# Optimization experiments

Hardware: AMD Instinct MI355X
Metric: run time of the kernel (lower is better)

## Reference

```python
import jax, jax.numpy as jnp
import numpy as np
from jax import lax

B, C, H, W, E = 16, 256, 64, 64, 4
KH = KW = 3
EPS = 1e-5  # torch BatchNorm2d default


def conv2d(x, w, groups=1):
    # x: [N, Cin, H, W], w: [Cout, Cin/groups, KH, KW], stride 1, pad 1 (autopad for k=3)
    return lax.conv_general_dilated(
        x, w, window_strides=(1, 1), padding=[(1, 1), (1, 1)],
        dimension_numbers=('NCHW', 'OIHW', 'NCHW'),
        feature_group_count=groups)


def bn(t, g, b, m, v):
    # eval-mode batchnorm over channel dim of [N, C, H, W]
    scale = g / jnp.sqrt(v + EPS)
    return (t - m[:, None, None]) * scale[:, None, None] + b[:, None, None]


def silu(t):
    return t * jax.nn.sigmoid(t)


def setup_inputs() -> dict:
    key = jax.random.key(0)
    ks = jax.random.split(key, 8)
    s = lambda k, sh: jax.random.normal(k, sh, jnp.float32) * 0.05
    return {
        'x': jax.random.normal(ks[0], (B, C, H, W), jnp.float32),
        # cv1: Conv(c1, c_, 3) = conv(no bias) + BN + SiLU
        'w1': s(ks[1], (C, C, KH, KW)),
        'bn1_g': jnp.ones((C,), jnp.float32),
        'bn1_b': jnp.zeros((C,), jnp.float32),
        'bn1_m': s(ks[2], (C,)),
        'bn1_v': jnp.abs(s(ks[3], (C,))) + 1.0,
        # cv2: DynamicConv routing linear (C -> E experts)
        'wr': s(ks[4], (E, C)),
        'br': jnp.zeros((E,), jnp.float32),
        # CondConv2d expert weight bank: [E, Cout*Cin*KH*KW]
        'w_e': s(ks[5], (E, C * C * KH * KW)),
        # cv2 BatchNorm2d
        'bn2_g': jnp.ones((C,), jnp.float32),
        'bn2_b': jnp.zeros((C,), jnp.float32),
        'bn2_m': s(ks[6], (C,)),
        'bn2_v': jnp.abs(s(ks[7], (C,))) + 1.0,
    }


def reference(x, w1, bn1_g, bn1_b, bn1_m, bn1_v, wr, br, w_e,
              bn2_g, bn2_b, bn2_m, bn2_v):
    # cv1: standard YOLO Conv (3x3, pad 1) + BN + SiLU
    y = silu(bn(conv2d(x, w1), bn1_g, bn1_b, bn1_m, bn1_v))  # [B, C, H, W]

    # DynamicConv_Single: global-avg-pool routing -> sigmoid gates over experts
    pooled = y.mean(axis=(2, 3))                       # [B, C]
    routing = jax.nn.sigmoid(pooled @ wr.T + br)       # [B, E]

    # CondConv2d: per-sample expert-weighted kernel, applied via batch-as-groups
    kern = (routing @ w_e).reshape(B * C, C, KH, KW)   # [B*Cout, Cin, 3, 3]
    yc = conv2d(y.reshape(1, B * C, H, W), kern, groups=B).reshape(B, C, H, W)

    # cv2 BN + SiLU, then residual add (shortcut and c1 == c2)
    out = silu(bn(yc, bn2_g, bn2_b, bn2_m, bn2_v))
    return x + out


if __name__ == '__main__':
    o = reference(**setup_inputs())
    print(o.shape, o.dtype)
```

## Files before the change

kernel.cpp:

```cpp
#include <hip/hip_runtime.h>
#include <math.h>

typedef _Float16 h16;
typedef _Float16 half8 __attribute__((ext_vector_type(8)));
typedef float f32x4 __attribute__((ext_vector_type(4)));

#define BATCH 16
#define CH 256
#define HH 64
#define WW 64
#define EPSBN 1e-5f

constexpr size_t WE_STRIDE = (size_t)CH * CH * 9;
constexpr int CIP = 40;
constexpr int XT_ELEMS = 4 * 66 * CIP;

__device__ __forceinline__ float silu_(float v) {
    return v * (1.0f / (1.0f + __expf(-v)));
}

template<int MODE>
__global__ __launch_bounds__(256, 3)
void conv_mfma(const void* __restrict__ inv,
               const h16* __restrict__ wt,
               const float* __restrict__ bng, const float* __restrict__ bnb,
               const float* __restrict__ bnm, const float* __restrict__ bnv,
               const float* __restrict__ resid,
               void* __restrict__ outv)
{
    __shared__ h16 xt[XT_ELEMS];

    const int t    = threadIdx.x;
    const int bx   = blockIdx.x;
    const int by   = blockIdx.y;
    const int bz   = blockIdx.z;
    const int h0   = bx * 2;
    const int co0  = by * 128;
    const int wv   = t >> 6;
    const int lane = t & 63;
    const int quad = lane >> 4;
    const int l15  = lane & 15;
    const int mh   = wv >> 1, nh = wv & 1;
    const int spHalf = (MODE == 0) ? mh : nh;
    const int coHalf = (MODE == 0) ? nh : mh;

    f32x4 acc[4][4];
    #pragma unroll
    for (int i = 0; i < 4; ++i)
        #pragma unroll
        for (int j = 0; j < 4; ++j) {
            f32x4 z = {0.f, 0.f, 0.f, 0.f};
            acc[i][j] = z;
        }

    const h16* wrow = wt + ((MODE == 1) ? (size_t)bz * 9 * 65536 : (size_t)0)
                         + ((size_t)(co0 + coHalf * 64 + l15) << 8)
                         + (size_t)(quad * 8);
    const int xbase = (spHalf * 66 + l15) * CIP + quad * 8;

    for (int ci0 = 0; ci0 < CH; ci0 += 32) {
        __syncthreads();
        if (MODE == 0) {
            const float* xin = (const float*)inv;
            for (int k = 0; k < 33; ++k) {
                int idx  = t + k * 256;
                int ci_i = idx / 264;
                int rem  = idx - ci_i * 264;
                int row  = rem / 66;
                int col  = rem - row * 66;
                int gh = h0 - 1 + row, gw = col - 1;
                float v = 0.f;
                if ((unsigned)gh < 64u && (unsigned)gw < 64u)
                    v = xin[((size_t)(bz * CH + ci0 + ci_i) << 12) + (gh << 6) + gw];
                xt[(row * 66 + col) * CIP + ci_i] = (h16)v;
            }
        } else {
            const h16* yin = (const h16*)inv;
            for (int k = 0; k < 5; ++k) {
                int idx = t + k * 256;
                if (idx < 1056) {
                    int cig = idx & 3;
                    int sp  = idx >> 2;
                    int row = sp / 66;
                    int col = sp - row * 66;
                    int gh = h0 - 1 + row, gw = col - 1;
                    half8 v = {0, 0, 0, 0, 0, 0, 0, 0};
                    if ((unsigned)gh < 64u && (unsigned)gw < 64u)
                        v = *(const half8*)(yin + (((size_t)(bz * 64 + gh) << 6) + gw) * 256
                                                + ci0 + cig * 8);
                    *(half8*)(xt + (row * 66 + col) * CIP + cig * 8) = v;
                }
            }
        }
        __syncthreads();

        const h16* wcol = wrow + ci0;
        #pragma unroll
        for (int kh = 0; kh < 3; ++kh)
        #pragma unroll
        for (int kw = 0; kw < 3; ++kw) {
            const int tap = kh * 3 + kw;
            half8 xf[4], wf[4];
            #pragma unroll
            for (int f = 0; f < 4; ++f) {
                xf[f] = *(const half8*)(xt + xbase + (kh * 66 + f * 16 + kw) * CIP);
                wf[f] = *(const half8*)(wcol + (size_t)tap * 65536 + f * 4096);
            }
            #pragma unroll
            for (int i = 0; i < 4; ++i)
                #pragma unroll
                for (int j = 0; j < 4; ++j) {
                    if (MODE == 0)
                        acc[i][j] = __builtin_amdgcn_mfma_f32_16x16x32_f16(
                            xf[i], wf[j], acc[i][j], 0, 0, 0);
                    else
                        acc[i][j] = __builtin_amdgcn_mfma_f32_16x16x32_f16(
                            wf[i], xf[j], acc[i][j], 0, 0, 0);
                }
        }
    }

    if (MODE == 0) {
        h16* yout = (h16*)outv;
        float sc[4], sh[4];
        #pragma unroll
        for (int j = 0; j < 4; ++j) {
            int c = co0 + coHalf * 64 + j * 16 + l15;
            float s = bng[c] * rsqrtf(bnv[c] + EPSBN);
            sc[j] = s; sh[j] = bnb[c] - bnm[c] * s;
        }
        #pragma unroll
        for (int i = 0; i < 4; ++i)
            #pragma unroll
            for (int r = 0; r < 4; ++r) {
                int spL = spHalf * 64 + i * 16 + quad * 4 + r;
                int h = h0 + (spL >> 6), w = spL & 63;
                size_t base = (((size_t)(bz * 64 + h) << 6) + w) * 256
                            + co0 + coHalf * 64 + l15;
                #pragma unroll
                for (int j = 0; j < 4; ++j) {
                    float v = acc[i][j][r] * sc[j] + sh[j];
                    yout[base + j * 16] = (h16)silu_(v);
                }
            }
    } else {
        float* outp = (float*)outv;
        #pragma unroll
        for (int i = 0; i < 4; ++i) {
            float sc[4], sh[4];
            #pragma unroll
            for (int r = 0; r < 4; ++r) {
                int c = co0 + coHalf * 64 + i * 16 + quad * 4 + r;
                float s = bng[c] * rsqrtf(bnv[c] + EPSBN);
                sc[r] = s; sh[r] = bnb[c] - bnm[c] * s;
            }
            #pragma unroll
            for (int j = 0; j < 4; ++j) {
                int spL = spHalf * 64 + j * 16 + l15;
                int h = h0 + (spL >> 6), w = spL & 63;
                #pragma unroll
                for (int r = 0; r < 4; ++r) {
                    int c = co0 + coHalf * 64 + i * 16 + quad * 4 + r;
                    size_t idx = ((size_t)(bz * CH + c) << 12) + (h << 6) + w;
                    float v = acc[i][j][r] * sc[r] + sh[r];
                    outp[idx] = resid[idx] + silu_(v);
                }
            }
        }
    }
}

__global__ void prep_w1(const float* __restrict__ w1, h16* __restrict__ w1t) {
    int pair = blockIdx.x * 256 + threadIdx.x;
    #pragma unroll
    for (int tap = 0; tap < 9; ++tap)
        w1t[((size_t)tap << 16) + pair] = (h16)w1[(size_t)pair * 9 + tap];
}

__global__ void pool_kernel(const h16* __restrict__ y, float* __restrict__ part) {
    int slice = blockIdx.x;
    int b     = blockIdx.y;
    int c     = threadIdx.x;
    const h16* p = y + ((size_t)b * 4096 + slice * 256) * 256 + c;
    float s = 0.f;
    #pragma unroll 8
    for (int i = 0; i < 256; ++i) s += (float)p[(size_t)i * 256];
    part[((size_t)slice * BATCH + b) * 256 + c] = s;
}

__global__ void routing_kernel(const float* __restrict__ part,
                               const float* __restrict__ wr,
                               const float* __restrict__ br,
                               float* __restrict__ routing) {
    int t = threadIdx.x;
    if (t < 64) {
        int b = t >> 2, e = t & 3;
        float s = 0.f;
        for (int c = 0; c < 256; ++c) {
            float p = 0.f;
            for (int sl = 0; sl < 16; ++sl)
                p += part[((size_t)sl * BATCH + b) * 256 + c];
            s += p * wr[e * 256 + c];
        }
        s = s * (1.f / 4096.f) + br[e];
        routing[t] = 1.f / (1.f + __expf(-s));
    }
}

__global__ void kern_gen(const float* __restrict__ w_e,
                         const float* __restrict__ routing,
                         h16* __restrict__ wt2) {
    __shared__ float rsh[64];
    int t = threadIdx.x;
    if (t < 64) rsh[t] = routing[t];
    __syncthreads();
    int pair = blockIdx.x * 256 + t;
    float wv[4][9];
    #pragma unroll
    for (int e = 0; e < 4; ++e)
        #pragma unroll
        for (int k = 0; k < 9; ++k)
            wv[e][k] = w_e[(size_t)e * WE_STRIDE + (size_t)pair * 9 + k];
    for (int b = 0; b < 16; ++b) {
        float r0 = rsh[b * 4 + 0], r1 = rsh[b * 4 + 1];
        float r2 = rsh[b * 4 + 2], r3 = rsh[b * 4 + 3];
        #pragma unroll
        for (int tap = 0; tap < 9; ++tap) {
            float s = r0 * wv[0][tap] + r1 * wv[1][tap]
                    + r2 * wv[2][tap] + r3 * wv[3][tap];
            wt2[((size_t)(b * 9 + tap) << 16) + pair] = (h16)s;
        }
    }
}

extern "C" void kernel_launch(void* const* d_in, const int* in_sizes, int n_in,
                              void* d_out, int out_size, void* d_ws, size_t ws_size,
                              hipStream_t stream) {
    const float* x    = (const float*)d_in[0];
    const float* w1   = (const float*)d_in[1];
    const float* bn1g = (const float*)d_in[2];
    const float* bn1b = (const float*)d_in[3];
    const float* bn1m = (const float*)d_in[4];
    const float* bn1v = (const float*)d_in[5];
    const float* wr   = (const float*)d_in[6];
    const float* br   = (const float*)d_in[7];
    const float* w_e  = (const float*)d_in[8];
    const float* bn2g = (const float*)d_in[9];
    const float* bn2b = (const float*)d_in[10];
    const float* bn2m = (const float*)d_in[11];
    const float* bn2v = (const float*)d_in[12];

    char* w = (char*)d_ws;
    h16*   y       = (h16*)(w);
    h16*   w1t     = (h16*)(w + 33554432);
    h16*   wt2     = (h16*)(w + 34734080);
    float* part    = (float*)(w + 53608448);
    float* routing = (float*)(w + 53870592);

    prep_w1<<<dim3(256), 256, 0, stream>>>(w1, w1t);

    dim3 cgrid(32, 2, BATCH);
    conv_mfma<0><<<cgrid, 256, 0, stream>>>(x, w1t, bn1g, bn1b, bn1m, bn1v,
                                            nullptr, y);
    pool_kernel<<<dim3(16, BATCH), 256, 0, stream>>>(y, part);
    routing_kernel<<<dim3(1), 64, 0, stream>>>(part, wr, br, routing);
    kern_gen<<<dim3(256), 256, 0, stream>>>(w_e, routing, wt2);
    conv_mfma<1><<<cgrid, 256, 0, stream>>>(y, wt2, bn2g, bn2b, bn2m, bn2v,
                                            x, (float*)d_out);
}
```

Baseline: 548.8 us.

## Pre-transpose input to NHWC fp16, re-tile conv warps, vectorize pool and kern_gen

Adds a prep_x kernel that transposes the fp32 NCHW input into an fp16 NHWC buffer, so the first conv stages its tile with vectorized half8 loads like the second conv. The LDS tile is reorganized into channel-group planes, and the warp tiling changes from 64x64 quadrants to each warp covering 32 output channels across all 128 spatial positions. The pool kernel reads half8 vectors and reduces through shared memory, and kern_gen stages expert weights through LDS with float4 loads for coalescing. The trade-off is an extra full-tensor transpose pass and a larger workspace, in exchange for removing the slow scalar strided gather in the first conv.

```diff
diff --git a/kernel.cpp b/kernel.cpp
--- a/kernel.cpp
+++ b/kernel.cpp
@@ -7,13 +7,10 @@
 
 #define BATCH 16
 #define CH 256
-#define HH 64
-#define WW 64
 #define EPSBN 1e-5f
 
 constexpr size_t WE_STRIDE = (size_t)CH * CH * 9;
-constexpr int CIP = 40;
-constexpr int XT_ELEMS = 4 * 66 * CIP;
+constexpr int REG = 2120;
 
 __device__ __forceinline__ float silu_(float v) {
     return v * (1.0f / (1.0f + __expf(-v)));
@@ -21,14 +18,14 @@
 
 template<int MODE>
 __global__ __launch_bounds__(256, 3)
-void conv_mfma(const void* __restrict__ inv,
+void conv_mfma(const h16* __restrict__ xin,
                const h16* __restrict__ wt,
                const float* __restrict__ bng, const float* __restrict__ bnb,
                const float* __restrict__ bnm, const float* __restrict__ bnv,
                const float* __restrict__ resid,
                void* __restrict__ outv)
 {
-    __shared__ h16 xt[XT_ELEMS];
+    __shared__ h16 xt[4 * REG];
 
     const int t    = threadIdx.x;
     const int bx   = blockIdx.x;
@@ -40,129 +37,113 @@
     const int lane = t & 63;
     const int quad = lane >> 4;
     const int l15  = lane & 15;
-    const int mh   = wv >> 1, nh = wv & 1;
-    const int spHalf = (MODE == 0) ? mh : nh;
-    const int coHalf = (MODE == 0) ? nh : mh;
-
-    f32x4 acc[4][4];
-    #pragma unroll
-    for (int i = 0; i < 4; ++i)
-        #pragma unroll
-        for (int j = 0; j < 4; ++j) {
-            f32x4 z = {0.f, 0.f, 0.f, 0.f};
-            acc[i][j] = z;
-        }
+
+    f32x4 acc[16];
+    #pragma unroll
+    for (int i = 0; i < 16; ++i) {
+        f32x4 z = {0.f, 0.f, 0.f, 0.f};
+        acc[i] = z;
+    }
 
     const h16* wrow = wt + ((MODE == 1) ? (size_t)bz * 9 * 65536 : (size_t)0)
-                         + ((size_t)(co0 + coHalf * 64 + l15) << 8)
+                         + ((size_t)(co0 + wv * 32 + l15) << 8)
                          + (size_t)(quad * 8);
-    const int xbase = (spHalf * 66 + l15) * CIP + quad * 8;
+    const h16* xlane = xt + quad * REG + l15 * 8;
 
     for (int ci0 = 0; ci0 < CH; ci0 += 32) {
         __syncthreads();
-        if (MODE == 0) {
-            const float* xin = (const float*)inv;
-            for (int k = 0; k < 33; ++k) {
-                int idx  = t + k * 256;
-                int ci_i = idx / 264;
-                int rem  = idx - ci_i * 264;
-                int row  = rem / 66;
-                int col  = rem - row * 66;
+        #pragma unroll
+        for (int k = 0; k < 5; ++k) {
+            int idx = t + k * 256;
+            if (idx < 1056) {
+                int cig = idx & 3;
+                int sp  = idx >> 2;
+                int row = sp / 66;
+                int col = sp - row * 66;
                 int gh = h0 - 1 + row, gw = col - 1;
-                float v = 0.f;
+                half8 v = {0, 0, 0, 0, 0, 0, 0, 0};
                 if ((unsigned)gh < 64u && (unsigned)gw < 64u)
-                    v = xin[((size_t)(bz * CH + ci0 + ci_i) << 12) + (gh << 6) + gw];
-                xt[(row * 66 + col) * CIP + ci_i] = (h16)v;
-            }
-        } else {
-            const h16* yin = (const h16*)inv;
-            for (int k = 0; k < 5; ++k) {
-                int idx = t + k * 256;
-                if (idx < 1056) {
-                    int cig = idx & 3;
-                    int sp  = idx >> 2;
-                    int row = sp / 66;
-                    int col = sp - row * 66;
-                    int gh = h0 - 1 + row, gw = col - 1;
-                    half8 v = {0, 0, 0, 0, 0, 0, 0, 0};
-                    if ((unsigned)gh < 64u && (unsigned)gw < 64u)
-                        v = *(const half8*)(yin + (((size_t)(bz * 64 + gh) << 6) + gw) * 256
-                                                + ci0 + cig * 8);
-                    *(half8*)(xt + (row * 66 + col) * CIP + cig * 8) = v;
-                }
+                    v = *(const half8*)(xin + (((size_t)(bz * 64 + gh) << 6) + gw) * 256
+                                            + ci0 + cig * 8);
+                *(half8*)(xt + cig * REG + sp * 8) = v;
             }
         }
         __syncthreads();
 
-        const h16* wcol = wrow + ci0;
+        const h16* wc = wrow + ci0;
         #pragma unroll
         for (int kh = 0; kh < 3; ++kh)
         #pragma unroll
         for (int kw = 0; kw < 3; ++kw) {
             const int tap = kh * 3 + kw;
-            half8 xf[4], wf[4];
-            #pragma unroll
-            for (int f = 0; f < 4; ++f) {
-                xf[f] = *(const half8*)(xt + xbase + (kh * 66 + f * 16 + kw) * CIP);
-                wf[f] = *(const half8*)(wcol + (size_t)tap * 65536 + f * 4096);
-            }
-            #pragma unroll
-            for (int i = 0; i < 4; ++i)
+            half8 wf[2], xf[8];
+            #pragma unroll
+            for (int f = 0; f < 2; ++f)
+                wf[f] = *(const half8*)(wc + (size_t)tap * 65536 + f * 4096);
+            #pragma unroll
+            for (int i = 0; i < 8; ++i)
+                xf[i] = *(const half8*)(xlane + ((kh + (i >> 2)) * 66 + (i & 3) * 16 + kw) * 8);
+            if (MODE == 0) {
                 #pragma unroll
-                for (int j = 0; j < 4; ++j) {
-                    if (MODE == 0)
-                        acc[i][j] = __builtin_amdgcn_mfma_f32_16x16x32_f16(
-                            xf[i], wf[j], acc[i][j], 0, 0, 0);
-                    else
-                        acc[i][j] = __builtin_amdgcn_mfma_f32_16x16x32_f16(
-                            wf[i], xf[j], acc[i][j], 0, 0, 0);
-                }
+                for (int i = 0; i < 8; ++i)
+                    #pragma unroll
+                    for (int j = 0; j < 2; ++j)
+                        acc[i * 2 + j] = __builtin_amdgcn_mfma_f32_16x16x32_f16(
+                            xf[i], wf[j], acc[i * 2 + j], 0, 0, 0);
+            } else {
+                #pragma unroll
+                for (int i = 0; i < 2; ++i)
+                    #pragma unroll
+                    for (int j = 0; j < 8; ++j)
+                        acc[i * 8 + j] = __builtin_amdgcn_mfma_f32_16x16x32_f16(
+                            wf[i], xf[j], acc[i * 8 + j], 0, 0, 0);
+            }
         }
     }
 
     if (MODE == 0) {
         h16* yout = (h16*)outv;
-        float sc[4], sh[4];
-        #pragma unroll
-        for (int j = 0; j < 4; ++j) {
-            int c = co0 + coHalf * 64 + j * 16 + l15;
+        float sc[2], sh[2];
+        #pragma unroll
+        for (int j = 0; j < 2; ++j) {
+            int c = co0 + wv * 32 + j * 16 + l15;
             float s = bng[c] * rsqrtf(bnv[c] + EPSBN);
             sc[j] = s; sh[j] = bnb[c] - bnm[c] * s;
         }
         #pragma unroll
-        for (int i = 0; i < 4; ++i)
+        for (int i = 0; i < 8; ++i)
             #pragma unroll
             for (int r = 0; r < 4; ++r) {
-                int spL = spHalf * 64 + i * 16 + quad * 4 + r;
+                int spL = i * 16 + quad * 4 + r;
                 int h = h0 + (spL >> 6), w = spL & 63;
                 size_t base = (((size_t)(bz * 64 + h) << 6) + w) * 256
-                            + co0 + coHalf * 64 + l15;
+                            + co0 + wv * 32 + l15;
                 #pragma unroll
-                for (int j = 0; j < 4; ++j) {
-                    float v = acc[i][j][r] * sc[j] + sh[j];
+                for (int j = 0; j < 2; ++j) {
+                    float v = acc[i * 2 + j][r] * sc[j] + sh[j];
                     yout[base + j * 16] = (h16)silu_(v);
                 }
             }
     } else {
         float* outp = (float*)outv;
         #pragma unroll
-        for (int i = 0; i < 4; ++i) {
+        for (int i = 0; i < 2; ++i) {
             float sc[4], sh[4];
             #pragma unroll
             for (int r = 0; r < 4; ++r) {
-                int c = co0 + coHalf * 64 + i * 16 + quad * 4 + r;
+                int c = co0 + wv * 32 + i * 16 + quad * 4 + r;
                 float s = bng[c] * rsqrtf(bnv[c] + EPSBN);
                 sc[r] = s; sh[r] = bnb[c] - bnm[c] * s;
             }
             #pragma unroll
-            for (int j = 0; j < 4; ++j) {
-                int spL = spHalf * 64 + j * 16 + l15;
+            for (int j = 0; j < 8; ++j) {
+                int spL = j * 16 + l15;
                 int h = h0 + (spL >> 6), w = spL & 63;
                 #pragma unroll
                 for (int r = 0; r < 4; ++r) {
-                    int c = co0 + coHalf * 64 + i * 16 + quad * 4 + r;
+                    int c = co0 + wv * 32 + i * 16 + quad * 4 + r;
                     size_t idx = ((size_t)(bz * CH + c) << 12) + (h << 6) + w;
-                    float v = acc[i][j][r] * sc[r] + sh[r];
+                    float v = acc[i * 8 + j][r] * sc[r] + sh[r];
                     outp[idx] = resid[idx] + silu_(v);
                 }
             }
@@ -170,6 +151,38 @@
     }
 }
 
+__global__ __launch_bounds__(256)
+void prep_x(const float* __restrict__ x, h16* __restrict__ xh) {
+    __shared__ float lt[64][65];
+    int cg = blockIdx.x, h = blockIdx.y, b = blockIdx.z;
+    int t = threadIdx.x;
+    {
+        int cl = t >> 2, wq = t & 3;
+        const float4* src = (const float4*)(x + (((size_t)(b * CH + cg * 64 + cl)) << 12)
+                                              + ((size_t)h << 6));
+        #pragma unroll
+        for (int k = 0; k < 4; ++k) {
+            int w4 = wq + k * 4;
+            float4 v = src[w4];
+            lt[cl][w4 * 4 + 0] = v.x;
+            lt[cl][w4 * 4 + 1] = v.y;
+            lt[cl][w4 * 4 + 2] = v.z;
+            lt[cl][w4 * 4 + 3] = v.w;
+        }
+    }
+    __syncthreads();
+    {
+        int wl = t >> 2, cq = t & 3;
+        half8 a2[2];
+        h16* ap = (h16*)a2;
+        #pragma unroll
+        for (int m = 0; m < 16; ++m) ap[m] = (h16)lt[cq * 16 + m][wl];
+        size_t base = ((((size_t)(b * 64 + h)) << 6) + wl) * 256 + cg * 64 + cq * 16;
+        *(half8*)(xh + base)     = a2[0];
+        *(half8*)(xh + base + 8) = a2[1];
+    }
+}
+
 __global__ void prep_w1(const float* __restrict__ w1, h16* __restrict__ w1t) {
     int pair = blockIdx.x * 256 + threadIdx.x;
     #pragma unroll
@@ -177,15 +190,29 @@
         w1t[((size_t)tap << 16) + pair] = (h16)w1[(size_t)pair * 9 + tap];
 }
 
-__global__ void pool_kernel(const h16* __restrict__ y, float* __restrict__ part) {
-    int slice = blockIdx.x;
-    int b     = blockIdx.y;
-    int c     = threadIdx.x;
-    const h16* p = y + ((size_t)b * 4096 + slice * 256) * 256 + c;
+__global__ __launch_bounds__(256)
+void pool_kernel(const h16* __restrict__ y, float* __restrict__ part) {
+    __shared__ float red[8][256];
+    int slice = blockIdx.x, b = blockIdx.y;
+    int t = threadIdx.x;
+    int oct = t & 31, ss = t >> 5;
+    float a[8];
+    #pragma unroll
+    for (int k = 0; k < 8; ++k) a[k] = 0.f;
+    const h16* p = y + ((size_t)(b * 4096 + slice * 256 + ss)) * 256 + oct * 8;
+    #pragma unroll 4
+    for (int i = 0; i < 32; ++i) {
+        half8 v = *(const half8*)(p + (size_t)i * 8 * 256);
+        #pragma unroll
+        for (int k = 0; k < 8; ++k) a[k] += (float)v[k];
+    }
+    #pragma unroll
+    for (int k = 0; k < 8; ++k) red[ss][oct * 8 + k] = a[k];
+    __syncthreads();
     float s = 0.f;
-    #pragma unroll 8
-    for (int i = 0; i < 256; ++i) s += (float)p[(size_t)i * 256];
-    part[((size_t)slice * BATCH + b) * 256 + c] = s;
+    #pragma unroll
+    for (int q = 0; q < 8; ++q) s += red[q][t];
+    part[((size_t)slice * BATCH + b) * 256 + t] = s;
 }
 
 __global__ void routing_kernel(const float* __restrict__ part,
@@ -207,20 +234,35 @@
     }
 }
 
-__global__ void kern_gen(const float* __restrict__ w_e,
-                         const float* __restrict__ routing,
-                         h16* __restrict__ wt2) {
+__global__ __launch_bounds__(256)
+void kern_gen(const float* __restrict__ w_e,
+              const float* __restrict__ routing,
+              h16* __restrict__ wt2) {
+    __shared__ float lw[4 * 2304];
     __shared__ float rsh[64];
     int t = threadIdx.x;
+    int pair0 = blockIdx.x * 256;
     if (t < 64) rsh[t] = routing[t];
+    #pragma unroll
+    for (int e = 0; e < 4; ++e) {
+        const float4* src = (const float4*)(w_e + (size_t)e * WE_STRIDE + (size_t)pair0 * 9);
+        #pragma unroll
+        for (int k = 0; k < 3; ++k) {
+            int idx = t + k * 256;
+            if (idx < 576) {
+                float4 v = src[idx];
+                float* d = &lw[e * 2304 + idx * 4];
+                d[0] = v.x; d[1] = v.y; d[2] = v.z; d[3] = v.w;
+            }
+        }
+    }
     __syncthreads();
-    int pair = blockIdx.x * 256 + t;
     float wv[4][9];
     #pragma unroll
     for (int e = 0; e < 4; ++e)
         #pragma unroll
         for (int k = 0; k < 9; ++k)
-            wv[e][k] = w_e[(size_t)e * WE_STRIDE + (size_t)pair * 9 + k];
+            wv[e][k] = lw[e * 2304 + t * 9 + k];
     for (int b = 0; b < 16; ++b) {
         float r0 = rsh[b * 4 + 0], r1 = rsh[b * 4 + 1];
         float r2 = rsh[b * 4 + 2], r3 = rsh[b * 4 + 3];
@@ -228,7 +270,7 @@
         for (int tap = 0; tap < 9; ++tap) {
             float s = r0 * wv[0][tap] + r1 * wv[1][tap]
                     + r2 * wv[2][tap] + r3 * wv[3][tap];
-            wt2[((size_t)(b * 9 + tap) << 16) + pair] = (h16)s;
+            wt2[((size_t)(b * 9 + tap) << 16) + pair0 + t] = (h16)s;
         }
     }
 }
@@ -251,16 +293,18 @@
     const float* bn2v = (const float*)d_in[12];
 
     char* w = (char*)d_ws;
-    h16*   y       = (h16*)(w);
-    h16*   w1t     = (h16*)(w + 33554432);
-    h16*   wt2     = (h16*)(w + 34734080);
-    float* part    = (float*)(w + 53608448);
-    float* routing = (float*)(w + 53870592);
-
+    h16*   xh      = (h16*)(w);
+    h16*   y       = (h16*)(w + 33554432);
+    h16*   w1t     = (h16*)(w + 67108864);
+    h16*   wt2     = (h16*)(w + 68288512);
+    float* part    = (float*)(w + 87162880);
+    float* routing = (float*)(w + 87425024);
+
+    prep_x<<<dim3(4, 64, BATCH), 256, 0, stream>>>(x, xh);
     prep_w1<<<dim3(256), 256, 0, stream>>>(w1, w1t);
 
     dim3 cgrid(32, 2, BATCH);
-    conv_mfma<0><<<cgrid, 256, 0, stream>>>(x, w1t, bn1g, bn1b, bn1m, bn1v,
+    conv_mfma<0><<<cgrid, 256, 0, stream>>>(xh, w1t, bn1g, bn1b, bn1m, bn1v,
                                             nullptr, y);
     pool_kernel<<<dim3(16, BATCH), 256, 0, stream>>>(y, part);
     routing_kernel<<<dim3(1), 64, 0, stream>>>(part, wr, br, routing);
```

Result: faster. 479.9 us (-12.6%).
